# Kernel tuning notes

Hardware: AMD Instinct MI355X
Metric: run time of the kernel (lower is better)

The kernel has to match this reference:

```python
import jax, jax.numpy as jnp
import numpy as np

D_MODEL = 1024  # scaling uses sqrt(d_model), as in the source


def setup_inputs() -> dict:
    key = jax.random.key(0)
    kx, kq, kk, kv = jax.random.split(key, 4)
    B, N, D, H = 4, 4096, D_MODEL, 128
    X = jax.random.normal(kx, (B, N, D), dtype=jnp.float32)
    # nn.Linear(d_model, d_head, bias=False) weights, stored as [d_model, d_head]
    s = 1.0 / np.sqrt(D)
    Wq = jax.random.normal(kq, (D, H), dtype=jnp.float32) * s
    Wk = jax.random.normal(kk, (D, H), dtype=jnp.float32) * s
    Wv = jax.random.normal(kv, (D, H), dtype=jnp.float32) * s
    return {"X": X, "Wq": Wq, "Wk": Wk, "Wv": Wv}


def reference(X, Wq, Wk, Wv):
    # Q, K, V: [B, N, H]
    Q = jnp.einsum("bnd,dh->bnh", X, Wq)
    K = jnp.einsum("bnd,dh->bnh", X, Wk)
    V = jnp.einsum("bnd,dh->bnh", X, Wv)
    # Scores: [B, N, N]; source divides by sqrt(d_model) (not sqrt(d_head))
    A = jnp.einsum("bqh,bkh->bqk", Q, K) / jnp.sqrt(jnp.float32(D_MODEL))
    A = jax.nn.softmax(A, axis=-1)
    # Dropout is identity in eval mode (deterministic reference baseline)
    return jnp.einsum("bqk,bkh->bqh", A, V)
```

## Files before the change

### kernel.cpp

```cpp
#include <hip/hip_runtime.h>
#include <stdint.h>

typedef __bf16 bf16_t;
typedef bf16_t bf16x8 __attribute__((ext_vector_type(8)));
typedef float f32x4 __attribute__((ext_vector_type(4)));
typedef float f32x16 __attribute__((ext_vector_type(16)));
typedef unsigned short u16;
typedef unsigned int u32;

#define MFMA16(a, b, c) __builtin_amdgcn_mfma_f32_16x16x32_bf16((a), (b), (c), 0, 0, 0)
#define MFMA32(a, b, c) __builtin_amdgcn_mfma_f32_32x32x16_bf16((a), (b), (c), 0, 0, 0)

#define QSCALE 0.04508422002778633f

__device__ __forceinline__ u16 f2bf(float f) {
  union { float f; unsigned u; } v; v.f = f;
  unsigned r = v.u + 0x7fffu + ((v.u >> 16) & 1u);
  return (u16)(r >> 16);
}

__device__ __forceinline__ void async_cp16(const void* g, void* l) {
  __builtin_amdgcn_global_load_lds(
      (__attribute__((address_space(1))) void*)(void*)g,
      (__attribute__((address_space(3))) void*)l, 16, 0, 0);
}

__device__ __forceinline__ u32 cvtpk(float lo, float hi) {
  u32 r;
  asm("v_cvt_pk_bf16_f32 %0, %1, %2" : "=v"(r) : "v"(lo), "v"(hi));
  return r;
}
__device__ __forceinline__ void pl32swap(u32& a, u32& b) {
  asm volatile("v_permlane32_swap_b32 %0, %1" : "+v"(a), "+v"(b));
}

__global__ __launch_bounds__(256) void pack_w_k(const float* __restrict__ Wq,
                                                const float* __restrict__ Wk,
                                                const float* __restrict__ Wv,
                                                u16* __restrict__ wp) {
  int t = blockIdx.x * 256 + threadIdx.x;
  int mat = t >> 14;
  int rr = t & 16383;
  int frag = rr >> 6, lane = rr & 63;
  int nt = frag >> 5, kc = frag & 31;
  const float* W = (mat == 0) ? Wq : ((mat == 1) ? Wk : Wv);
  int k0 = kc * 32 + ((lane >> 4) << 3);
  int col = nt * 16 + (lane & 15);
  union { u16 h[8]; uint4 q; } u_;
#pragma unroll
  for (int j = 0; j < 8; ++j) u_.h[j] = f2bf(W[(size_t)(k0 + j) * 128 + col]);
  *(uint4*)(wp + (size_t)t * 8) = u_.q;
}

__global__ __launch_bounds__(256) void qkv_k(const float* __restrict__ X,
                                             const u16* __restrict__ wp,
                                             u16* __restrict__ Qb,
                                             u16* __restrict__ Kb,
                                             u16* __restrict__ Vt) {
  __shared__ __align__(16) u16 xs[2048];
  const int tid = threadIdx.x;
  const int w = tid >> 6, lane = tid & 63;
  const int r16 = lane >> 4, c16 = lane & 15;
  const int m0 = blockIdx.x * 32;

  f32x4 acc[2][6];
#pragma unroll
  for (int mt = 0; mt < 2; ++mt)
#pragma unroll
    for (int i = 0; i < 6; ++i) acc[mt][i] = (f32x4){0.f, 0.f, 0.f, 0.f};

  const int srow = tid >> 3, scol = tid & 7;
  const float* sbase = X + (size_t)(m0 + srow) * 1024 + scol * 8;
  const int soff = srow * 128 + ((scol * 16) ^ ((srow & 7) << 4));

  for (int kc = 0; kc < 16; ++kc) {
    float4 v0 = *(const float4*)(sbase + kc * 64);
    float4 v1 = *(const float4*)(sbase + kc * 64 + 4);
    union { u16 h[8]; uint4 q; } u_;
    u_.h[0] = f2bf(v0.x); u_.h[1] = f2bf(v0.y); u_.h[2] = f2bf(v0.z); u_.h[3] = f2bf(v0.w);
    u_.h[4] = f2bf(v1.x); u_.h[5] = f2bf(v1.y); u_.h[6] = f2bf(v1.z); u_.h[7] = f2bf(v1.w);
    *(uint4*)((char*)xs + soff) = u_.q;
    __syncthreads();
    bf16x8 a[2][2];
#pragma unroll
    for (int mt = 0; mt < 2; ++mt)
#pragma unroll
      for (int ks = 0; ks < 2; ++ks) {
        int row = mt * 16 + c16;
        int off = row * 128 + (((ks * 64) + r16 * 16) ^ ((row & 7) << 4));
        a[mt][ks] = *(const bf16x8*)((const char*)xs + off);
      }
#pragma unroll
    for (int i = 0; i < 6; ++i) {
      int t = w + 4 * i;
      int mat = t >> 3, nt = t & 7;
      const u16* bp = wp + (size_t)mat * 131072 +
                      (size_t)((nt * 32 + kc * 2) * 64 + lane) * 8;
#pragma unroll
      for (int ks = 0; ks < 2; ++ks) {
        bf16x8 b = *(const bf16x8*)(bp + (size_t)ks * 512);
#pragma unroll
        for (int mt = 0; mt < 2; ++mt) acc[mt][i] = MFMA16(a[mt][ks], b, acc[mt][i]);
      }
    }
    __syncthreads();
  }

  const int batch = m0 >> 12;
#pragma unroll
  for (int i = 0; i < 6; ++i) {
    int t = w + 4 * i;
    int mat = t >> 3, nt = t & 7;
#pragma unroll
    for (int mt = 0; mt < 2; ++mt) {
      f32x4 v = acc[mt][i];
      if (mat == 2) {
        int d = nt * 16 + c16;
        int nloc = (m0 & 4095) + mt * 16 + r16 * 4;
        union { u16 h[4]; uint2 q; } u_;
#pragma unroll
        for (int r = 0; r < 4; ++r) u_.h[r] = f2bf(v[r]);
        *(uint2*)(Vt + ((size_t)(batch * 128 + d)) * 4096 + nloc) = u_.q;
      } else {
        u16* dstm = (mat == 0) ? Qb : Kb;
        float sc = (mat == 0) ? QSCALE : 1.0f;
#pragma unroll
        for (int r = 0; r < 4; ++r) {
          int row = m0 + mt * 16 + r16 * 4 + r;
          dstm[(size_t)row * 128 + nt * 16 + c16] = f2bf(v[r] * sc);
        }
      }
    }
  }
}

__device__ __forceinline__ void attn_stage(const char* kp, const char* vp,
                                           char* smem, int buf, int tid) {
  char* kd = smem + buf * 16384;
  char* vd = smem + 32768 + buf * 16384;
#pragma unroll
  for (int i = 0; i < 4; ++i) {
    int s = i * 4096 + tid * 16;
    int row = s >> 8, cb = s & 255;
    async_cp16(kp + (size_t)row * 256 + (cb ^ ((row & 15) << 4)), kd + s);
  }
#pragma unroll
  for (int i = 0; i < 4; ++i) {
    int s = i * 4096 + tid * 16;
    int d = s >> 7, cb = s & 127;
    async_cp16(vp + (size_t)d * 8192 + (cb ^ ((d & 7) << 4)), vd + s);
  }
}

__global__ __launch_bounds__(256, 2) void attn_k(const u16* __restrict__ Qb,
                                                 const u16* __restrict__ Kb,
                                                 const u16* __restrict__ Vt,
                                                 float* __restrict__ Opart,
                                                 float2* __restrict__ Ml,
                                                 int nsplit, int chunk) {
  __shared__ __align__(16) char smem[65536];
  const int tid = threadIdx.x;
  const int w = tid >> 6, lane = tid & 63;
  const int l31 = lane & 31, hi = lane >> 5;

  const int B = gridDim.x;
  int xcd = blockIdx.x & 7, idx = blockIdx.x >> 3;
  int linear = xcd * (B >> 3) + idx;
  int g = linear >> 5, qt = linear & 31;
  int batch = g / nsplit, split = g - batch * nsplit;
  const int q0 = qt * 128;
  const int n0 = split * chunk;
  const int T = chunk >> 6;

  const char* kbase = (const char*)Kb + ((size_t)batch * 4096 + n0) * 256;
  const char* vbase = (const char*)Vt + (size_t)batch * 1048576 + (size_t)n0 * 2;

  bf16x8 qf[8];
  const u16* qrow = Qb + ((size_t)batch * 4096 + q0 + w * 32 + l31) * 128 + hi * 8;
#pragma unroll
  for (int kc = 0; kc < 8; ++kc) qf[kc] = *(const bf16x8*)(qrow + kc * 16);

  f32x16 acc[4];
#pragma unroll
  for (int dt = 0; dt < 4; ++dt)
#pragma unroll
    for (int j = 0; j < 16; ++j) acc[dt][j] = 0.f;
  float mr = -3.0e38f, lr = 0.f;
  const int swzK = (lane & 15) << 4;
  const int swzV = (lane & 7) << 4;

  attn_stage(kbase, vbase, smem, 0, tid);

  for (int t = 0; t < T; ++t) {
    if (t + 1 < T) {
      attn_stage(kbase + (size_t)(t + 1) * 16384, vbase + (size_t)(t + 1) * 128,
                 smem, (t + 1) & 1, tid);
      asm volatile("s_waitcnt vmcnt(8)" ::: "memory");
    } else {
      asm volatile("s_waitcnt vmcnt(0)" ::: "memory");
    }
    __builtin_amdgcn_s_barrier();
    asm volatile("" ::: "memory");
    const char* kb = smem + (t & 1) * 16384;
    const char* vb = smem + 32768 + (t & 1) * 16384;

    f32x16 sv[2];
    __builtin_amdgcn_s_setprio(1);
#pragma unroll
    for (int nt = 0; nt < 2; ++nt) {
      f32x16 s = {};
      const char* krow = kb + (nt * 32 + l31) * 256;
#pragma unroll
      for (int kc = 0; kc < 8; ++kc) {
        bf16x8 kf = *(const bf16x8*)(krow + ((kc * 32 + hi * 16) ^ swzK));
        s = MFMA32(kf, qf[kc], s);
      }
      sv[nt] = s;
    }
    __builtin_amdgcn_s_setprio(0);

    float m16[16];
#pragma unroll
    for (int i = 0; i < 16; ++i) m16[i] = fmaxf(sv[0][i], sv[1][i]);
#pragma unroll
    for (int st = 8; st > 0; st >>= 1)
#pragma unroll
      for (int i = 0; i < st; ++i) m16[i] = fmaxf(m16[i], m16[i + st]);
    float mx = fmaxf(m16[0], __shfl_xor(m16[0], 32));
    float mold = mr;
    float mnew = (mx > mold + 11.5f) ? mx : mold;
    mr = mnew;

    float pr[2][16];
#pragma unroll
    for (int nt = 0; nt < 2; ++nt)
#pragma unroll
      for (int i = 0; i < 16; ++i) pr[nt][i] = exp2f(sv[nt][i] - mnew);
    float s16[16];
#pragma unroll
    for (int i = 0; i < 16; ++i) s16[i] = pr[0][i] + pr[1][i];
#pragma unroll
    for (int st = 8; st > 0; st >>= 1)
#pragma unroll
      for (int i = 0; i < st; ++i) s16[i] += s16[i + st];
    float rs = s16[0] + __shfl_xor(s16[0], 32);

    if (__any(mnew > mold)) {
      float a_ = exp2f(mold - mnew);
      lr *= a_;
#pragma unroll
      for (int r = 0; r < 16; ++r) {
        float aq = __shfl(a_, ((r & 3) + 8 * (r >> 2)) + 4 * hi);
#pragma unroll
        for (int dt = 0; dt < 4; ++dt) acc[dt][r] *= aq;
      }
    }
    lr += rs;

    bf16x8 pf[4];
#pragma unroll
    for (int nt = 0; nt < 2; ++nt)
#pragma unroll
      for (int half = 0; half < 2; ++half) {
        const float* p = &pr[nt][half * 8];
        u32 a0 = cvtpk(p[0], p[1]);
        u32 b0 = cvtpk(p[4], p[5]);
        u32 c0 = cvtpk(p[2], p[3]);
        u32 d0 = cvtpk(p[6], p[7]);
        pl32swap(a0, b0);
        pl32swap(c0, d0);
        union { u32 u[4]; bf16x8 v; } pu;
        pu.u[0] = a0; pu.u[1] = c0; pu.u[2] = b0; pu.u[3] = d0;
        pf[nt * 2 + half] = pu.v;
      }

    __builtin_amdgcn_s_setprio(1);
#pragma unroll
    for (int dt = 0; dt < 4; ++dt) {
      const char* vrow = vb + (dt * 32 + l31) * 128;
#pragma unroll
      for (int ks = 0; ks < 4; ++ks) {
        bf16x8 vf = *(const bf16x8*)(vrow + ((ks * 32 + hi * 16) ^ swzV));
        acc[dt] = MFMA32(pf[ks], vf, acc[dt]);
      }
    }
    __builtin_amdgcn_s_setprio(0);

    asm volatile("" ::: "memory");
    __builtin_amdgcn_s_barrier();
    asm volatile("" ::: "memory");
  }

  size_t obase = (size_t)split * 16384 + (size_t)batch * 4096 + q0 + w * 32;
#pragma unroll
  for (int dt = 0; dt < 4; ++dt)
#pragma unroll
    for (int r = 0; r < 16; ++r) {
      int qr = (r & 3) + 8 * (r >> 2) + 4 * hi;
      Opart[(obase + qr) * 128 + dt * 32 + l31] = acc[dt][r];
    }
  if (lane < 32)
    Ml[split * 16384 + batch * 4096 + q0 + w * 32 + lane] = make_float2(mr, lr);
}

__global__ __launch_bounds__(256) void reduce_k(const float* __restrict__ Op,
                                                const float2* __restrict__ Ml,
                                                float* __restrict__ Out, int S) {
  int t = blockIdx.x * 256 + threadIdx.x;
  int q = t >> 5, d4 = (t & 31) << 2;
  float ms[4], ls[4];
  float M = -3.0e38f;
  for (int s = 0; s < S; ++s) {
    float2 v = Ml[s * 16384 + q];
    ms[s] = v.x; ls[s] = v.y;
    M = fmaxf(M, v.x);
  }
  float L = 0.f, o0 = 0.f, o1 = 0.f, o2 = 0.f, o3 = 0.f;
  for (int s = 0; s < S; ++s) {
    float wgt = exp2f(ms[s] - M);
    L += ls[s] * wgt;
    float4 pv = *(const float4*)(Op + ((size_t)s * 16384 + q) * 128 + d4);
    o0 += pv.x * wgt; o1 += pv.y * wgt; o2 += pv.z * wgt; o3 += pv.w * wgt;
  }
  float inv = 1.0f / L;
  float4 r = {o0 * inv, o1 * inv, o2 * inv, o3 * inv};
  *(float4*)(Out + (size_t)q * 128 + d4) = r;
}

extern "C" void kernel_launch(void* const* d_in, const int* in_sizes, int n_in,
                              void* d_out, int out_size, void* d_ws, size_t ws_size,
                              hipStream_t stream) {
  const float* X  = (const float*)d_in[0];
  const float* Wq = (const float*)d_in[1];
  const float* Wk = (const float*)d_in[2];
  const float* Wv = (const float*)d_in[3];
  float* Out = (float*)d_out;
  char* ws = (char*)d_ws;
  u16* Qb = (u16*)(ws);
  u16* Kb = (u16*)(ws + (4u << 20));
  u16* Vt = (u16*)(ws + (8u << 20));
  u16* Wp = (u16*)(ws + (12u << 20));
  const size_t pbase = 13631488ull;
  int S = 1;
  if (ws_size >= pbase + 4ull * 8519680ull) S = 4;
  else if (ws_size >= pbase + 2ull * 8519680ull) S = 2;
  float* Opart = (float*)(ws + pbase);
  float2* Ml   = (float2*)(ws + pbase + (size_t)S * 8388608ull);

  pack_w_k<<<dim3(192), dim3(256), 0, stream>>>(Wq, Wk, Wv, Wp);
  qkv_k<<<dim3(512), dim3(256), 0, stream>>>(X, Wp, Qb, Kb, Vt);
  attn_k<<<dim3(128 * S), dim3(256), 0, stream>>>(Qb, Kb, Vt, Opart, Ml, S, 4096 / S);
  reduce_k<<<dim3(2048), dim3(256), 0, stream>>>(Opart, Ml, Out, S);
}
```

Baseline: 96.66 us.

## Prepack K/V into MFMA fragment order, use 512-thread blocks, fp16 partials, split-8

Adds a pass that rearranges K and V into per-tile MFMA fragment order, so the attention kernel's async loads become contiguous copies and its LDS reads become plain lane-strided loads with no XOR swizzle. The attention kernel moves to 512-thread blocks covering 256 queries, allowing up to eight KV splits. Partial outputs are normalised and stored as fp16 to halve traffic, and the reduce is templated on the split count. Fast exp2/rcp intrinsics are also used. The cost is an extra kernel launch plus a K/V copy, and lower precision in the partial sums.

After: 151.5 us. +56.8%, slower.

```diff
diff --git a/kernel.cpp b/kernel.cpp
--- a/kernel.cpp
+++ b/kernel.cpp
@@ -17,6 +17,22 @@
   union { float f; unsigned u; } v; v.f = f;
   unsigned r = v.u + 0x7fffu + ((v.u >> 16) & 1u);
   return (u16)(r >> 16);
+}
+
+__device__ __forceinline__ float exp2x(float x) {
+#if __has_builtin(__builtin_amdgcn_exp2f)
+  return __builtin_amdgcn_exp2f(x);
+#else
+  return exp2f(x);
+#endif
+}
+
+__device__ __forceinline__ float rcpx(float x) {
+#if __has_builtin(__builtin_amdgcn_rcpf)
+  return __builtin_amdgcn_rcpf(x);
+#else
+  return 1.0f / x;
+#endif
 }
 
 __device__ __forceinline__ void async_cp16(const void* g, void* l) {
@@ -134,28 +150,44 @@
   }
 }
 
-__device__ __forceinline__ void attn_stage(const char* kp, const char* vp,
-                                           char* smem, int buf, int tid) {
+__global__ __launch_bounds__(256) void pack_kv_k(const u16* __restrict__ Kb,
+                                                 const u16* __restrict__ Vt,
+                                                 u16* __restrict__ Kf,
+                                                 u16* __restrict__ Vf) {
+  int t = blockIdx.x * 256 + threadIdx.x;
+  int lane = t & 63, l31 = lane & 31, hi = (lane >> 5) & 1;
+  if (t < 262144) {
+    int frag = t >> 6;
+    int batch = frag >> 10, kt = (frag >> 3) & 127, kc = frag & 7;
+    const u16* src = Kb + ((size_t)batch * 4096 + kt * 32 + l31) * 128 + kc * 16 + hi * 8;
+    *(uint4*)(Kf + (size_t)t * 8) = *(const uint4*)src;
+  } else {
+    int o = t - 262144;
+    int frag = o >> 6;
+    int batch = frag >> 10, tt = (frag >> 4) & 63, ks = (frag >> 2) & 3, dt = frag & 3;
+    const u16* src = Vt + ((size_t)batch * 128 + dt * 32 + l31) * 4096 + tt * 64 + ks * 16 + hi * 8;
+    *(uint4*)(Vf + (size_t)o * 8) = *(const uint4*)src;
+  }
+}
+
+__device__ __forceinline__ void attn_stage(const char* kfc, const char* vfc,
+                                           char* smem, int t, int buf, int tid) {
   char* kd = smem + buf * 16384;
   char* vd = smem + 32768 + buf * 16384;
-#pragma unroll
-  for (int i = 0; i < 4; ++i) {
-    int s = i * 4096 + tid * 16;
-    int row = s >> 8, cb = s & 255;
-    async_cp16(kp + (size_t)row * 256 + (cb ^ ((row & 15) << 4)), kd + s);
-  }
-#pragma unroll
-  for (int i = 0; i < 4; ++i) {
-    int s = i * 4096 + tid * 16;
-    int d = s >> 7, cb = s & 127;
-    async_cp16(vp + (size_t)d * 8192 + (cb ^ ((d & 7) << 4)), vd + s);
-  }
-}
-
-__global__ __launch_bounds__(256, 2) void attn_k(const u16* __restrict__ Qb,
-                                                 const u16* __restrict__ Kb,
-                                                 const u16* __restrict__ Vt,
-                                                 float* __restrict__ Opart,
+  const char* ks = kfc + (size_t)t * 16384;
+  const char* vs = vfc + (size_t)t * 16384;
+#pragma unroll
+  for (int i = 0; i < 2; ++i)
+    async_cp16(ks + i * 8192 + tid * 16, kd + i * 8192 + tid * 16);
+#pragma unroll
+  for (int i = 0; i < 2; ++i)
+    async_cp16(vs + i * 8192 + tid * 16, vd + i * 8192 + tid * 16);
+}
+
+__global__ __launch_bounds__(512, 4) void attn_k(const u16* __restrict__ Qb,
+                                                 const u16* __restrict__ Kf,
+                                                 const u16* __restrict__ Vf,
+                                                 _Float16* __restrict__ Opart,
                                                  float2* __restrict__ Ml,
                                                  int nsplit, int chunk) {
   __shared__ __align__(16) char smem[65536];
@@ -166,14 +198,14 @@
   const int B = gridDim.x;
   int xcd = blockIdx.x & 7, idx = blockIdx.x >> 3;
   int linear = xcd * (B >> 3) + idx;
-  int g = linear >> 5, qt = linear & 31;
+  int qt = linear & 15, g = linear >> 4;
   int batch = g / nsplit, split = g - batch * nsplit;
-  const int q0 = qt * 128;
+  const int q0 = qt * 256;
   const int n0 = split * chunk;
   const int T = chunk >> 6;
 
-  const char* kbase = (const char*)Kb + ((size_t)batch * 4096 + n0) * 256;
-  const char* vbase = (const char*)Vt + (size_t)batch * 1048576 + (size_t)n0 * 2;
+  const char* kfc = (const char*)Kf + (size_t)batch * 1048576 + (size_t)(n0 >> 6) * 16384;
+  const char* vfc = (const char*)Vf + (size_t)batch * 1048576 + (size_t)(n0 >> 6) * 16384;
 
   bf16x8 qf[8];
   const u16* qrow = Qb + ((size_t)batch * 4096 + q0 + w * 32 + l31) * 128 + hi * 8;
@@ -186,16 +218,13 @@
 #pragma unroll
     for (int j = 0; j < 16; ++j) acc[dt][j] = 0.f;
   float mr = -3.0e38f, lr = 0.f;
-  const int swzK = (lane & 15) << 4;
-  const int swzV = (lane & 7) << 4;
-
-  attn_stage(kbase, vbase, smem, 0, tid);
+
+  attn_stage(kfc, vfc, smem, 0, 0, tid);
 
   for (int t = 0; t < T; ++t) {
     if (t + 1 < T) {
-      attn_stage(kbase + (size_t)(t + 1) * 16384, vbase + (size_t)(t + 1) * 128,
-                 smem, (t + 1) & 1, tid);
-      asm volatile("s_waitcnt vmcnt(8)" ::: "memory");
+      attn_stage(kfc, vfc, smem, t + 1, (t + 1) & 1, tid);
+      asm volatile("s_waitcnt vmcnt(4)" ::: "memory");
     } else {
       asm volatile("s_waitcnt vmcnt(0)" ::: "memory");
     }
@@ -209,10 +238,9 @@
 #pragma unroll
     for (int nt = 0; nt < 2; ++nt) {
       f32x16 s = {};
-      const char* krow = kb + (nt * 32 + l31) * 256;
 #pragma unroll
       for (int kc = 0; kc < 8; ++kc) {
-        bf16x8 kf = *(const bf16x8*)(krow + ((kc * 32 + hi * 16) ^ swzK));
+        bf16x8 kf = *(const bf16x8*)(kb + (nt * 8 + kc) * 1024 + lane * 16);
         s = MFMA32(kf, qf[kc], s);
       }
       sv[nt] = s;
@@ -235,7 +263,7 @@
 #pragma unroll
     for (int nt = 0; nt < 2; ++nt)
 #pragma unroll
-      for (int i = 0; i < 16; ++i) pr[nt][i] = exp2f(sv[nt][i] - mnew);
+      for (int i = 0; i < 16; ++i) pr[nt][i] = exp2x(sv[nt][i] - mnew);
     float s16[16];
 #pragma unroll
     for (int i = 0; i < 16; ++i) s16[i] = pr[0][i] + pr[1][i];
@@ -246,7 +274,7 @@
     float rs = s16[0] + __shfl_xor(s16[0], 32);
 
     if (__any(mnew > mold)) {
-      float a_ = exp2f(mold - mnew);
+      float a_ = exp2x(mold - mnew);
       lr *= a_;
 #pragma unroll
       for (int r = 0; r < 16; ++r) {
@@ -277,10 +305,9 @@
     __builtin_amdgcn_s_setprio(1);
 #pragma unroll
     for (int dt = 0; dt < 4; ++dt) {
-      const char* vrow = vb + (dt * 32 + l31) * 128;
 #pragma unroll
       for (int ks = 0; ks < 4; ++ks) {
-        bf16x8 vf = *(const bf16x8*)(vrow + ((ks * 32 + hi * 16) ^ swzV));
+        bf16x8 vf = *(const bf16x8*)(vb + (ks * 4 + dt) * 1024 + lane * 16);
         acc[dt] = MFMA32(pf[ks], vf, acc[dt]);
       }
     }
@@ -297,34 +324,44 @@
 #pragma unroll
     for (int r = 0; r < 16; ++r) {
       int qr = (r & 3) + 8 * (r >> 2) + 4 * hi;
-      Opart[(obase + qr) * 128 + dt * 32 + l31] = acc[dt][r];
+      float lq = __shfl(lr, qr);
+      Opart[(obase + qr) * 128 + dt * 32 + l31] = (_Float16)(acc[dt][r] * rcpx(lq));
     }
   if (lane < 32)
-    Ml[split * 16384 + batch * 4096 + q0 + w * 32 + lane] = make_float2(mr, lr);
-}
-
-__global__ __launch_bounds__(256) void reduce_k(const float* __restrict__ Op,
+    Ml[(size_t)split * 16384 + (size_t)batch * 4096 + q0 + w * 32 + lane] =
+        make_float2(mr, lr);
+}
+
+template <int S>
+__global__ __launch_bounds__(256) void reduce_k(const _Float16* __restrict__ Op,
                                                 const float2* __restrict__ Ml,
-                                                float* __restrict__ Out, int S) {
+                                                float* __restrict__ Out) {
   int t = blockIdx.x * 256 + threadIdx.x;
-  int q = t >> 5, d4 = (t & 31) << 2;
-  float ms[4], ls[4];
+  int q = t >> 4, d8 = (t & 15) << 3;
+  float ms[S], ls[S];
   float M = -3.0e38f;
+#pragma unroll
   for (int s = 0; s < S; ++s) {
-    float2 v = Ml[s * 16384 + q];
+    float2 v = Ml[(size_t)s * 16384 + q];
     ms[s] = v.x; ls[s] = v.y;
     M = fmaxf(M, v.x);
   }
-  float L = 0.f, o0 = 0.f, o1 = 0.f, o2 = 0.f, o3 = 0.f;
+  float L = 0.f;
+  float o[8] = {0.f, 0.f, 0.f, 0.f, 0.f, 0.f, 0.f, 0.f};
+#pragma unroll
   for (int s = 0; s < S; ++s) {
-    float wgt = exp2f(ms[s] - M);
-    L += ls[s] * wgt;
-    float4 pv = *(const float4*)(Op + ((size_t)s * 16384 + q) * 128 + d4);
-    o0 += pv.x * wgt; o1 += pv.y * wgt; o2 += pv.z * wgt; o3 += pv.w * wgt;
-  }
-  float inv = 1.0f / L;
-  float4 r = {o0 * inv, o1 * inv, o2 * inv, o3 * inv};
-  *(float4*)(Out + (size_t)q * 128 + d4) = r;
+    float wgt = exp2x(ms[s] - M) * ls[s];
+    L += wgt;
+    union { uint4 u; _Float16 h[8]; } pv;
+    pv.u = *(const uint4*)(Op + ((size_t)s * 16384 + q) * 128 + d8);
+#pragma unroll
+    for (int j = 0; j < 8; ++j) o[j] += (float)pv.h[j] * wgt;
+  }
+  float inv = rcpx(L);
+  float4 r0 = {o[0] * inv, o[1] * inv, o[2] * inv, o[3] * inv};
+  float4 r1 = {o[4] * inv, o[5] * inv, o[6] * inv, o[7] * inv};
+  *(float4*)(Out + (size_t)q * 128 + d8) = r0;
+  *(float4*)(Out + (size_t)q * 128 + d8 + 4) = r1;
 }
 
 extern "C" void kernel_launch(void* const* d_in, const int* in_sizes, int n_in,
@@ -337,18 +374,22 @@
   float* Out = (float*)d_out;
   char* ws = (char*)d_ws;
   u16* Qb = (u16*)(ws);
-  u16* Kb = (u16*)(ws + (4u << 20));
-  u16* Vt = (u16*)(ws + (8u << 20));
-  u16* Wp = (u16*)(ws + (12u << 20));
-  const size_t pbase = 13631488ull;
-  int S = 1;
-  if (ws_size >= pbase + 4ull * 8519680ull) S = 4;
-  else if (ws_size >= pbase + 2ull * 8519680ull) S = 2;
-  float* Opart = (float*)(ws + pbase);
-  float2* Ml   = (float2*)(ws + pbase + (size_t)S * 8388608ull);
+  u16* Kf = (u16*)(ws + (4u << 20));
+  u16* Vf = (u16*)(ws + (8u << 20));
+  _Float16* Opart = (_Float16*)(ws + (12u << 20));
+  u16* Kb = (u16*)(ws + (12u << 20));
+  u16* Vt = (u16*)(ws + (16u << 20));
+  u16* Wp = (u16*)(ws + (20u << 20));
+
+  int S = (ws_size >= (12ull << 20) + 8ull * 4325376ull) ? 8 : 4;
+  float2* Ml = (float2*)(ws + (12ull << 20) + (size_t)S * 4194304ull);
 
   pack_w_k<<<dim3(192), dim3(256), 0, stream>>>(Wq, Wk, Wv, Wp);
   qkv_k<<<dim3(512), dim3(256), 0, stream>>>(X, Wp, Qb, Kb, Vt);
-  attn_k<<<dim3(128 * S), dim3(256), 0, stream>>>(Qb, Kb, Vt, Opart, Ml, S, 4096 / S);
-  reduce_k<<<dim3(2048), dim3(256), 0, stream>>>(Opart, Ml, Out, S);
-}
+  pack_kv_k<<<dim3(2048), dim3(256), 0, stream>>>(Kb, Vt, Kf, Vf);
+  attn_k<<<dim3(64 * S), dim3(512), 0, stream>>>(Qb, Kf, Vf, Opart, Ml, S, 4096 / S);
+  if (S == 8)
+    reduce_k<8><<<dim3(1024), dim3(256), 0, stream>>>(Opart, Ml, Out);
+  else
+    reduce_k<4><<<dim3(1024), dim3(256), 0, stream>>>(Opart, Ml, Out);
+}
```
